# Kernel optimization log

Measured on AMD Instinct MI355X. Metric: run time of the kernel, lower is better.

The kernel has to match this reference:

```python
import jax, jax.numpy as jnp
import numpy as np

N = 100_000      # nodes
E = 1_600_000    # edges
IN = 128         # input_dim
HID = 64         # hidden_dim
H = 4            # num_heads
DH = HID // H    # per-head dim
L = 3            # num_layers
OUT = 64         # output_dim
SLOPE = 0.2      # DGL GATConv LeakyReLU default
EPS = 1e-5       # LayerNorm eps


def setup_inputs() -> dict:
    key = jax.random.key(0)
    ks = jax.random.split(key, 20)
    s = 0.02
    return {
        "node_features": jax.random.normal(ks[0], (N, IN), jnp.float32),
        "src": jax.random.randint(ks[1], (E,), 0, N, jnp.int32),
        "dst": jax.random.randint(ks[2], (E,), 0, N, jnp.int32),
        # input projection
        "W_in": jax.random.normal(ks[3], (IN, HID), jnp.float32) * s,
        "b_in": jnp.zeros((HID,), jnp.float32),
        # rewiring MLP: Linear(2*HID,64) -> Tanh -> Linear(64,1) -> Sigmoid
        "W_a1": jax.random.normal(ks[4], (2 * HID, 64), jnp.float32) * s,
        "b_a1": jnp.zeros((64,), jnp.float32),
        "W_a2": jax.random.normal(ks[5], (64, 1), jnp.float32) * s,
        "b_a2": jnp.zeros((1,), jnp.float32),
        # stacked GATConv params for L layers
        "W_gat": jax.random.normal(ks[6], (L, HID, H * DH), jnp.float32) * s,
        "a_l": jax.random.normal(ks[7], (L, H, DH), jnp.float32) * s,
        "a_r": jax.random.normal(ks[8], (L, H, DH), jnp.float32) * s,
        "b_gat": jnp.zeros((L, H, DH), jnp.float32),
        # LayerNorm + output projection
        "ln_g": jnp.ones((HID,), jnp.float32),
        "ln_b": jnp.zeros((HID,), jnp.float32),
        "W_out": jax.random.normal(ks[9], (HID, OUT), jnp.float32) * s,
        "b_out": jnp.zeros((OUT,), jnp.float32),
    }


def _gat_layer(h, src, dst, W, al, ar, b):
    # h: (N, HID) -> z: (N, H, DH)
    z = (h @ W).reshape(N, H, DH)
    el = jnp.sum(z * al, axis=-1)                       # (N, H)
    er = jnp.sum(z * ar, axis=-1)                       # (N, H)
    e = jax.nn.leaky_relu(el[src] + er[dst], SLOPE)     # (E, H)
    # segment softmax over incoming edges of each dst node
    m = jax.ops.segment_max(e, dst, num_segments=N)     # (N, H)
    ex = jnp.exp(e - m[dst])                            # (E, H)
    den = jax.ops.segment_sum(ex, dst, num_segments=N)  # (N, H)
    alpha = ex / den[dst]                               # (E, H)
    msg = z[src] * alpha[..., None]                     # (E, H, DH)
    out = jax.ops.segment_sum(msg, dst, num_segments=N) # (N, H, DH)
    # residual (identity since HID == H*DH) + bias, then flatten(1)
    out = out + h.reshape(N, H, DH) + b
    return out.reshape(N, H * DH)


def reference(node_features, src, dst, W_in, b_in, W_a1, b_a1, W_a2, b_a2,
              W_gat, a_l, a_r, b_gat, ln_g, ln_b, W_out, b_out):
    h = node_features @ W_in + b_in                     # (N, HID)
    # GraphRewiringModule: edge-wise gather + MLP + sigmoid score
    he = jnp.concatenate([h[src], h[dst]], axis=1)      # (E, 2*HID)
    edge_score = jax.nn.sigmoid(jnp.tanh(he @ W_a1 + b_a1) @ W_a2 + b_a2)  # (E,1); unused downstream, as in source
    for l in range(L):
        h = _gat_layer(h, src, dst, W_gat[l], a_l[l], a_r[l], b_gat[l])
    # LayerNorm
    mu = jnp.mean(h, axis=-1, keepdims=True)
    var = jnp.mean((h - mu) ** 2, axis=-1, keepdims=True)
    h = (h - mu) * jax.lax.rsqrt(var + EPS) * ln_g + ln_b
    return h @ W_out + b_out                            # (N, OUT)
```

## Files before the change

kernel.cpp:

```cpp
#include <hip/hip_runtime.h>

#define NN 100000
#define EE 1600000
#define IN_DIM 128
#define HID 64
#define NH 4
#define DH 16
#define NL 3
#define OUT_DIM 64
#define SLOPE 0.2f
#define LN_EPS 1e-5f
#define RB 4
#define ZSC 64.0f
#define ZISC 0.015625f

#define BSH 9
#define BSZ 512
#define NB ((NN + BSZ - 1) / BSZ)
#define CAP 10240
#define CHUNK 4096
#define P1_BLOCKS ((EE + CHUNK - 1) / CHUNK)

using short8 = __attribute__((ext_vector_type(8))) short;
using f32x4  = __attribute__((ext_vector_type(4))) float;
using f32x2  = __attribute__((ext_vector_type(2))) float;

__device__ __forceinline__ float bcast(float x, int lane) {
    return __int_as_float(__builtin_amdgcn_readlane(__float_as_int(x), lane));
}
__device__ __forceinline__ unsigned f2bf(float x) {
    unsigned u = __float_as_uint(x);
    u += 0x7FFFu + ((u >> 16) & 1u);
    return u >> 16;
}
__device__ __forceinline__ float bf2f(unsigned short b) {
    return __uint_as_float(((unsigned)b) << 16);
}
__device__ __forceinline__ float bflo(unsigned zp) {
    return __uint_as_float(zp << 16);
}
__device__ __forceinline__ float bfhi(unsigned zp) {
    return __uint_as_float(zp & 0xFFFF0000u);
}

__global__ void k_wpack(const float* __restrict__ W, uint4* __restrict__ Wb) {
    const int tid = blockIdx.x * 256 + threadIdx.x;
    if (tid >= 1024) return;
    const int lane = tid & 63;
    const int ntkk = tid >> 6;
    const int nt = ntkk & 3, kk = ntkk >> 2;
    const int k0 = kk * 32 + (lane >> 4) * 8;
    const int n  = nt * 16 + (lane & 15);
    unsigned dw[4];
#pragma unroll
    for (int p = 0; p < 4; ++p) {
        const unsigned lo = f2bf(W[(k0 + 2 * p) * HID + n]);
        const unsigned hi = f2bf(W[(k0 + 2 * p + 1) * HID + n]);
        dw[p] = lo | (hi << 16);
    }
    Wb[ntkk * 64 + lane] = make_uint4(dw[0], dw[1], dw[2], dw[3]);
}

__device__ float walv(const float* __restrict__ W, const float* __restrict__ al,
                      const float* __restrict__ ar, int k, int c) {
    if (c < 4) {
        float s = 0.f;
#pragma unroll
        for (int d = 0; d < 16; ++d) s += W[k * HID + c * 16 + d] * al[c * 16 + d];
        return s;
    }
    if (c < 8) {
        const int hh = c - 4;
        float s = 0.f;
#pragma unroll
        for (int d = 0; d < 16; ++d) s += W[k * HID + hh * 16 + d] * ar[hh * 16 + d];
        return s;
    }
    return 0.f;
}

__global__ void k_wpack_gat(const float* __restrict__ W_gat, const float* __restrict__ a_l,
                            const float* __restrict__ a_r, uint4* __restrict__ Wbg) {
    const int l = blockIdx.y;
    const int tid = blockIdx.x * 256 + threadIdx.x;
    if (tid >= 640) return;
    const int lane = tid & 63;
    const int f = tid >> 6;
    const int kk = f / 5, nt = f % 5;
    const float* W  = W_gat + (size_t)l * HID * HID;
    const float* al = a_l + (size_t)l * HID;
    const float* ar = a_r + (size_t)l * HID;
    const int k0 = kk * 32 + (lane >> 4) * 8;
    const int n  = lane & 15;
    unsigned dw[4];
#pragma unroll
    for (int p = 0; p < 4; ++p) {
        float b0, b1;
        if (nt < 4) {
            b0 = W[(k0 + 2 * p) * HID + nt * 16 + n];
            b1 = W[(k0 + 2 * p + 1) * HID + nt * 16 + n];
        } else {
            b0 = walv(W, al, ar, k0 + 2 * p, n);
            b1 = walv(W, al, ar, k0 + 2 * p + 1, n);
        }
        dw[p] = f2bf(b0) | (f2bf(b1) << 16);
    }
    Wbg[(size_t)l * 640 + f * 64 + lane] = make_uint4(dw[0], dw[1], dw[2], dw[3]);
}

__global__ __launch_bounds__(256)
void k_in_gemm(const float* __restrict__ X, const uint4* __restrict__ Wb,
               const float* __restrict__ b, unsigned* __restrict__ h32) {
    const int l  = threadIdx.x & 63;
    const int wv = threadIdx.x >> 6;
    const int wrow = blockIdx.x * 64 + wv * 16;
    if (wrow >= NN) return;
    const int arow = wrow + (l & 15);
    const int kb_off = (l >> 4) * 8;
    f32x4 acc[4];
#pragma unroll
    for (int nt = 0; nt < 4; ++nt) acc[nt] = (f32x4){0.f, 0.f, 0.f, 0.f};
    const float* xr = X + (size_t)arow * IN_DIM;
#pragma unroll
    for (int kk = 0; kk < 4; ++kk) {
        const int kb = kk * 32 + kb_off;
        const float4 xa = *(const float4*)(xr + kb);
        const float4 xb = *(const float4*)(xr + kb + 4);
        const unsigned d0 = f2bf(xa.x) | (f2bf(xa.y) << 16);
        const unsigned d1 = f2bf(xa.z) | (f2bf(xa.w) << 16);
        const unsigned d2 = f2bf(xb.x) | (f2bf(xb.y) << 16);
        const unsigned d3 = f2bf(xb.z) | (f2bf(xb.w) << 16);
        const uint4 au = make_uint4(d0, d1, d2, d3);
        const short8 af = __builtin_bit_cast(short8, au);
#pragma unroll
        for (int nt = 0; nt < 4; ++nt) {
            const uint4 bu = Wb[(kk * 4 + nt) * 64 + l];
            const short8 bf = __builtin_bit_cast(short8, bu);
            acc[nt] = __builtin_amdgcn_mfma_f32_16x16x32_bf16(af, bf, acc[nt], 0, 0, 0);
        }
    }
    const int grp = l >> 4, ci = l & 15;
#pragma unroll
    for (int nt = 0; nt < 4; ++nt) {
        const float bv = b[nt * 16 + ci];
#pragma unroll
        for (int r = 0; r < 4; ++r) {
            const int row = wrow + grp * 4 + r;
            const unsigned my = f2bf(acc[nt][r] + bv);
            const unsigned ot = (unsigned)__shfl_xor((int)my, 1, 64);
            if ((ci & 1) == 0)
                h32[(size_t)row * 32 + nt * 8 + (ci >> 1)] = my | (ot << 16);
        }
    }
}

__global__ __launch_bounds__(256)
void k_zgemm(const unsigned short* __restrict__ h16, const uint4* __restrict__ Wbg,
             unsigned* __restrict__ zb8, float* __restrict__ el, float* __restrict__ er) {
    const int l  = threadIdx.x & 63;
    const int wv = threadIdx.x >> 6;
    const int wrow = blockIdx.x * 64 + wv * 16;
    if (wrow >= NN) return;
    const int arow = wrow + (l & 15);
    const int kb_off = (l >> 4) * 8;
    f32x4 acc[5];
#pragma unroll
    for (int nt = 0; nt < 5; ++nt) acc[nt] = (f32x4){0.f, 0.f, 0.f, 0.f};
#pragma unroll
    for (int kk = 0; kk < 2; ++kk) {
        const int kb = kk * 32 + kb_off;
        const uint4 au = *(const uint4*)(h16 + (size_t)arow * 64 + kb);
        const short8 af = __builtin_bit_cast(short8, au);
#pragma unroll
        for (int nt = 0; nt < 5; ++nt) {
            const uint4 bu = Wbg[(kk * 5 + nt) * 64 + l];
            const short8 bf = __builtin_bit_cast(short8, bu);
            acc[nt] = __builtin_amdgcn_mfma_f32_16x16x32_bf16(af, bf, acc[nt], 0, 0, 0);
        }
    }
    const int grp = l >> 4, ci = l & 15;
#pragma unroll
    for (int nt = 0; nt < 4; ++nt) {
#pragma unroll
        for (int r = 0; r < 4; ++r) {
            const int row = wrow + grp * 4 + r;
            const float v = acc[nt][r] * ZSC;
            const float vn = __shfl_xor(v, 1, 64);
            unsigned pk = (unsigned)__builtin_amdgcn_cvt_pk_fp8_f32(v, vn, 0, false) & 0xFFFFu;
            const unsigned pk2 = (unsigned)__shfl_xor((int)pk, 2, 64);
            pk |= pk2 << 16;
            if ((ci & 3) == 0)
                zb8[(size_t)row * 16 + nt * 4 + (ci >> 2)] = pk;
        }
    }
#pragma unroll
    for (int r = 0; r < 4; ++r) {
        const int row = wrow + grp * 4 + r;
        const float v = acc[4][r];
        if (ci < 4) el[row * NH + ci] = v;
        else if (ci < 8) er[row * NH + (ci - 4)] = v;
    }
}


__global__ void k_zero_bcnt(int* __restrict__ bcnt, int* __restrict__ esrc_pad) {
    if (threadIdx.x < NB) bcnt[threadIdx.x] = 0;
    if (threadIdx.x < 32) esrc_pad[threadIdx.x] = 0;
}

__global__ __launch_bounds__(256)
void k_bucketize(const int* __restrict__ src, const int* __restrict__ dst,
                 int* __restrict__ bcnt, unsigned* __restrict__ bbuf) {
    __shared__ int lh[256];
    __shared__ int lbase[256];
    __shared__ int lcnt[256];
    __shared__ int gbase[256];
    __shared__ int sc[256];
    __shared__ int2 stage[CHUNK];
    const int t = threadIdx.x;
    const int e0 = blockIdx.x * CHUNK;
    const int n = min(CHUNK, EE - e0);
    lh[t] = 0;
    __syncthreads();
    int myd[CHUNK / 256], mys[CHUNK / 256];
#pragma unroll
    for (int i = 0; i < CHUNK / 256; ++i) {
        const int o = i * 256 + t;
        if (o < n) {
            myd[i] = dst[e0 + o];
            mys[i] = src[e0 + o];
            atomicAdd(&lh[myd[i] >> BSH], 1);
        } else myd[i] = -1;
    }
    __syncthreads();
    {
        const int v = lh[t];
        lcnt[t] = v;
        sc[t] = v;
        __syncthreads();
        for (int off = 1; off < 256; off <<= 1) {
            const int x = (t >= off) ? sc[t - off] : 0;
            __syncthreads();
            sc[t] += x;
            __syncthreads();
        }
        lbase[t] = sc[t] - v;
        lh[t] = sc[t] - v;
    }
    __syncthreads();
#pragma unroll
    for (int i = 0; i < CHUNK / 256; ++i) {
        if (myd[i] >= 0) {
            const int b = myd[i] >> BSH;
            const int p = atomicAdd(&lh[b], 1);
            stage[p] = make_int2(mys[i], myd[i]);
        }
    }
    __syncthreads();
    if (t < NB && lcnt[t] > 0) gbase[t] = atomicAdd(&bcnt[t], lcnt[t]);
    __syncthreads();
    for (int i = t; i < n; i += 256) {
        const int2 en = stage[i];
        const int b = en.y >> BSH;
        const int gp = gbase[b] + (i - lbase[b]);
        if (gp < CAP)
            bbuf[(size_t)b * CAP + gp] =
                (unsigned)en.x | (((unsigned)en.y & 511u) << 17);
    }
}

__global__ void k_bscan(const int* __restrict__ bcnt, int* __restrict__ bbase,
                        int* __restrict__ rowptr) {
    const int t = threadIdx.x;
    __shared__ int sc[256];
    const int v = (t < NB) ? bcnt[t] : 0;
    sc[t] = v;
    __syncthreads();
    for (int off = 1; off < 256; off <<= 1) {
        const int x = (t >= off) ? sc[t - off] : 0;
        __syncthreads();
        sc[t] += x;
        __syncthreads();
    }
    if (t < NB) bbase[t] = sc[t] - v;
    if (t == 0) rowptr[NN] = EE;
}

__global__ __launch_bounds__(256)
void k_localcsr(const int* __restrict__ bcnt, const int* __restrict__ bbase,
                const unsigned* __restrict__ bbuf, int* __restrict__ rowptr,
                int* __restrict__ esrc) {
    const int b = blockIdx.x;
    const int t = threadIdx.x;
    const int cnt = bcnt[b];
    const int base = bbase[b];
    const int n0 = b * BSZ;
    const int nn = min(BSZ, NN - n0);
    __shared__ int lh[BSZ];
    __shared__ int lsc[BSZ];
    __shared__ int sc[256];
    for (int i = t; i < BSZ; i += 256) lh[i] = 0;
    __syncthreads();
    const unsigned* bb = bbuf + (size_t)b * CAP;
    for (int i = t; i < cnt; i += 256) atomicAdd(&lh[(bb[i] >> 17) & 511u], 1);
    __syncthreads();
    const int a0 = lh[2 * t], a1 = lh[2 * t + 1];
    const int ts = a0 + a1;
    sc[t] = ts;
    __syncthreads();
    for (int off = 1; off < 256; off <<= 1) {
        const int x = (t >= off) ? sc[t - off] : 0;
        __syncthreads();
        sc[t] += x;
        __syncthreads();
    }
    const int ebase = sc[t] - ts;
    lsc[2 * t] = ebase;
    lsc[2 * t + 1] = ebase + a0;
    __syncthreads();
    for (int i = t; i < BSZ; i += 256) {
        if (i < nn) rowptr[n0 + i] = base + lsc[i];
        lh[i] = lsc[i];
    }
    __syncthreads();
    for (int i = t; i < cnt; i += 256) {
        const unsigned en = bb[i];
        const int p = atomicAdd(&lh[(en >> 17) & 511u], 1);
        esrc[base + p] = (int)(en & 0x1FFFFu);
    }
}

__global__ __launch_bounds__(256)
void k_gat_dst(const int* __restrict__ rowptr, const int* __restrict__ esrc,
               const float* __restrict__ el, const float* __restrict__ er,
               const uint2* __restrict__ zb64, const unsigned short* __restrict__ hin16,
               const float* __restrict__ bg, unsigned* __restrict__ hout32) {
    const int j  = threadIdx.x & 63;
    const int wv = threadIdx.x >> 6;
    const int d = blockIdx.x * 4 + wv;
    if (d >= NN) return;
    const int g = j >> 3;
    const int q = j & 7;
    const int hh = q >> 1;
    const int r0 = rowptr[d], r1 = rowptr[d + 1];
    const float erh = er[d * NH + hh];
    uint4 hv4 = make_uint4(0, 0, 0, 0);
    if (g == 0) hv4 = *(const uint4*)(hin16 + (size_t)d * 64 + 8 * q);
    float a0 = 0.f, a1 = 0.f, a2 = 0.f, a3 = 0.f;
    float a4 = 0.f, a5 = 0.f, a6 = 0.f, a7 = 0.f;
    float den = 0.f;
    unsigned sA = (unsigned)esrc[r0 + g];
    float avA = el[sA * NH + hh];
    uint2 zpA = zb64[sA * 8u + q];
    unsigned sB = (unsigned)esrc[r0 + 8 + g];
    for (int i = r0; i < r1; i += 8) {
        const float avB = el[sB * NH + hh];
        const uint2 zpB = zb64[sB * 8u + q];
        const unsigned sC = (unsigned)esrc[i + 16 + g];
        const float x = avA + erh;
        float w = __expf(fmaxf(x, SLOPE * x));
        w = (i + g < r1) ? w : 0.f;
        den += w;
        const f32x2 p0 = __builtin_amdgcn_cvt_pk_f32_fp8(zpA.x, false);
        const f32x2 p1 = __builtin_amdgcn_cvt_pk_f32_fp8(zpA.x, true);
        const f32x2 p2 = __builtin_amdgcn_cvt_pk_f32_fp8(zpA.y, false);
        const f32x2 p3 = __builtin_amdgcn_cvt_pk_f32_fp8(zpA.y, true);
        a0 = fmaf(w, p0.x, a0);
        a1 = fmaf(w, p0.y, a1);
        a2 = fmaf(w, p1.x, a2);
        a3 = fmaf(w, p1.y, a3);
        a4 = fmaf(w, p2.x, a4);
        a5 = fmaf(w, p2.y, a5);
        a6 = fmaf(w, p3.x, a6);
        a7 = fmaf(w, p3.y, a7);
        sA = sB; avA = avB; zpA = zpB; sB = sC;
    }
#pragma unroll
    for (int m = 8; m <= 32; m <<= 1) {
        den += __shfl_xor(den, m, 64);
        a0 += __shfl_xor(a0, m, 64);
        a1 += __shfl_xor(a1, m, 64);
        a2 += __shfl_xor(a2, m, 64);
        a3 += __shfl_xor(a3, m, 64);
        a4 += __shfl_xor(a4, m, 64);
        a5 += __shfl_xor(a5, m, 64);
        a6 += __shfl_xor(a6, m, 64);
        a7 += __shfl_xor(a7, m, 64);
    }
    if (g == 0) {
        const int c = 8 * q;
        float o0 = bflo(hv4.x) + bg[c + 0], o1 = bfhi(hv4.x) + bg[c + 1];
        float o2 = bflo(hv4.y) + bg[c + 2], o3 = bfhi(hv4.y) + bg[c + 3];
        float o4 = bflo(hv4.z) + bg[c + 4], o5 = bfhi(hv4.z) + bg[c + 5];
        float o6 = bflo(hv4.w) + bg[c + 6], o7 = bfhi(hv4.w) + bg[c + 7];
        if (r1 > r0) {
            const float rds = (1.f / den) * ZISC;
            o0 = fmaf(a0, rds, o0); o1 = fmaf(a1, rds, o1);
            o2 = fmaf(a2, rds, o2); o3 = fmaf(a3, rds, o3);
            o4 = fmaf(a4, rds, o4); o5 = fmaf(a5, rds, o5);
            o6 = fmaf(a6, rds, o6); o7 = fmaf(a7, rds, o7);
        }
        const uint4 ov = make_uint4(f2bf(o0) | (f2bf(o1) << 16),
                                    f2bf(o2) | (f2bf(o3) << 16),
                                    f2bf(o4) | (f2bf(o5) << 16),
                                    f2bf(o6) | (f2bf(o7) << 16));
        *(uint4*)(hout32 + (size_t)d * 32 + 4 * q) = ov;
    }
}

__global__ __launch_bounds__(256, 4)
void k_ln_out(const unsigned short* __restrict__ h16, const float* __restrict__ g,
              const float* __restrict__ be, const float* __restrict__ Wo,
              const float* __restrict__ bo, float* __restrict__ out) {
    const int j = threadIdx.x & 63;
    float Wreg[HID];
#pragma unroll
    for (int k = 0; k < HID; ++k) Wreg[k] = Wo[k * OUT_DIM + j];
    const float gj = g[j], bej = be[j], boj = bo[j];
    const int wid = (blockIdx.x * blockDim.x + threadIdx.x) >> 6;
    const int nw  = (gridDim.x * blockDim.x) >> 6;
    for (int v0 = wid * RB; v0 < NN; v0 += nw * RB) {
        float hn[RB];
#pragma unroll
        for (int r = 0; r < RB; ++r) {
            const float x = bf2f(h16[(size_t)(v0 + r) * HID + j]);
            float s = x;
#pragma unroll
            for (int m = 32; m >= 1; m >>= 1) s += __shfl_xor(s, m, 64);
            const float mu = s * (1.f / 64.f);
            const float dx = x - mu;
            float vs = dx * dx;
#pragma unroll
            for (int m = 32; m >= 1; m >>= 1) vs += __shfl_xor(vs, m, 64);
            hn[r] = dx * rsqrtf(vs * (1.f / 64.f) + LN_EPS) * gj + bej;
        }
        float acc[RB];
#pragma unroll
        for (int r = 0; r < RB; ++r) acc[r] = boj;
#pragma unroll
        for (int k = 0; k < HID; ++k) {
#pragma unroll
            for (int r = 0; r < RB; ++r)
                acc[r] = fmaf(bcast(hn[r], k), Wreg[k], acc[r]);
        }
#pragma unroll
        for (int r = 0; r < RB; ++r) out[(size_t)(v0 + r) * OUT_DIM + j] = acc[r];
    }
}

extern "C" void kernel_launch(void* const* d_in, const int* in_sizes, int n_in,
                              void* d_out, int out_size, void* d_ws, size_t ws_size,
                              hipStream_t stream) {
    const float* X     = (const float*)d_in[0];
    const int*   src   = (const int*)d_in[1];
    const int*   dst   = (const int*)d_in[2];
    const float* W_in  = (const float*)d_in[3];
    const float* b_in  = (const float*)d_in[4];
    const float* W_gat = (const float*)d_in[9];
    const float* a_l   = (const float*)d_in[10];
    const float* a_r   = (const float*)d_in[11];
    const float* b_gat = (const float*)d_in[12];
    const float* ln_g  = (const float*)d_in[13];
    const float* ln_b  = (const float*)d_in[14];
    const float* W_out = (const float*)d_in[15];
    const float* b_out = (const float*)d_in[16];
    float* out = (float*)d_out;

    char* ws = (char*)d_ws;
    unsigned short* hA16 = (unsigned short*)ws;
    unsigned short* hB16 = hA16 + (size_t)NN * HID;
    unsigned* zb8 = (unsigned*)(hB16 + (size_t)NN * HID);
    float* el = (float*)(zb8 + (size_t)NN * 16);
    float* er = el + (size_t)NN * NH;
    int* rowptr = (int*)(er + (size_t)NN * NH);
    int* esrc   = rowptr + NN + 1;
    int* bcnt   = esrc + EE + 32;
    int* bbase  = bcnt + NB;
    uintptr_t wp = (uintptr_t)(bbase + NB);
    wp = (wp + 15) & ~(uintptr_t)15;
    uint4* Wb   = (uint4*)wp;
    uint4* Wbg  = Wb + 1024;
    unsigned* bbuf = (unsigned*)hB16;

    k_wpack<<<4, 256, 0, stream>>>(W_in, Wb);
    k_wpack_gat<<<dim3(3, NL), 256, 0, stream>>>(W_gat, a_l, a_r, Wbg);
    k_in_gemm<<<(NN + 63) / 64, 256, 0, stream>>>(X, Wb, b_in, (unsigned*)hA16);

    k_zero_bcnt<<<1, 256, 0, stream>>>(bcnt, esrc + EE);
    k_bucketize<<<P1_BLOCKS, 256, 0, stream>>>(src, dst, bcnt, bbuf);
    k_bscan<<<1, 256, 0, stream>>>(bcnt, bbase, rowptr);
    k_localcsr<<<NB, 256, 0, stream>>>(bcnt, bbase, bbuf, rowptr, esrc);

    unsigned short* hin = hA16;
    unsigned short* hout = hB16;
    for (int l = 0; l < NL; ++l) {
        k_zgemm<<<(NN + 63) / 64, 256, 0, stream>>>(hin, Wbg + (size_t)l * 640,
                                                    zb8, el, er);
        k_gat_dst<<<(NN + 3) / 4, 256, 0, stream>>>(rowptr, esrc, el, er,
                                                    (const uint2*)zb8, hin,
                                                    b_gat + (size_t)l * HID,
                                                    (unsigned*)hout);
        unsigned short* t = hin; hin = hout; hout = t;
    }

    k_ln_out<<<1024, 256, 0, stream>>>(hin, ln_g, ln_b, W_out, b_out, out);
}
```

Before: 296.0 us.

## Recompute source attention logits from fp8 z in gather; shrink bucketize staging

The GAT aggregation kernel no longer gathers a precomputed el value per edge. It recomputes el inside the edge loop as a dot product of the already-loaded fp8 z row with a_l, plus one lane shuffle. This removes one random 4-byte gather per edge and the el writes from the z-GEMM. The cost is extra ALU work per edge, and el is now computed from quantized fp8 z instead of the fp32 GEMM output, which lowers accuracy. Separately, the bucketize staging buffer stores the packed 32-bit edge word plus a byte-sized bucket id instead of an int2, cutting LDS use.

```diff
diff --git a/kernel.cpp b/kernel.cpp
--- a/kernel.cpp
+++ b/kernel.cpp
@@ -156,7 +156,7 @@
 
 __global__ __launch_bounds__(256)
 void k_zgemm(const unsigned short* __restrict__ h16, const uint4* __restrict__ Wbg,
-             unsigned* __restrict__ zb8, float* __restrict__ el, float* __restrict__ er) {
+             unsigned* __restrict__ zb8, float* __restrict__ er) {
     const int l  = threadIdx.x & 63;
     const int wv = threadIdx.x >> 6;
     const int wrow = blockIdx.x * 64 + wv * 16;
@@ -197,8 +197,7 @@
     for (int r = 0; r < 4; ++r) {
         const int row = wrow + grp * 4 + r;
         const float v = acc[4][r];
-        if (ci < 4) el[row * NH + ci] = v;
-        else if (ci < 8) er[row * NH + (ci - 4)] = v;
+        if (ci >= 4 && ci < 8) er[row * NH + (ci - 4)] = v;
     }
 }
 
@@ -216,7 +215,8 @@
     __shared__ int lcnt[256];
     __shared__ int gbase[256];
     __shared__ int sc[256];
-    __shared__ int2 stage[CHUNK];
+    __shared__ unsigned stage[CHUNK];
+    __shared__ unsigned char sbkt[CHUNK];
     const int t = threadIdx.x;
     const int e0 = blockIdx.x * CHUNK;
     const int n = min(CHUNK, EE - e0);
@@ -253,19 +253,17 @@
         if (myd[i] >= 0) {
             const int b = myd[i] >> BSH;
             const int p = atomicAdd(&lh[b], 1);
-            stage[p] = make_int2(mys[i], myd[i]);
+            stage[p] = (unsigned)mys[i] | (((unsigned)myd[i] & 511u) << 17);
+            sbkt[p] = (unsigned char)b;
         }
     }
     __syncthreads();
     if (t < NB && lcnt[t] > 0) gbase[t] = atomicAdd(&bcnt[t], lcnt[t]);
     __syncthreads();
     for (int i = t; i < n; i += 256) {
-        const int2 en = stage[i];
-        const int b = en.y >> BSH;
+        const int b = sbkt[i];
         const int gp = gbase[b] + (i - lbase[b]);
-        if (gp < CAP)
-            bbuf[(size_t)b * CAP + gp] =
-                (unsigned)en.x | (((unsigned)en.y & 511u) << 17);
+        if (gp < CAP) bbuf[(size_t)b * CAP + gp] = stage[i];
     }
 }
 
@@ -332,7 +330,7 @@
 
 __global__ __launch_bounds__(256)
 void k_gat_dst(const int* __restrict__ rowptr, const int* __restrict__ esrc,
-               const float* __restrict__ el, const float* __restrict__ er,
+               const float* __restrict__ al, const float* __restrict__ er,
                const uint2* __restrict__ zb64, const unsigned short* __restrict__ hin16,
                const float* __restrict__ bg, unsigned* __restrict__ hout32) {
     const int j  = threadIdx.x & 63;
@@ -344,27 +342,30 @@
     const int hh = q >> 1;
     const int r0 = rowptr[d], r1 = rowptr[d + 1];
     const float erh = er[d * NH + hh];
+    const float4 alA = *(const float4*)(al + 8 * q);
+    const float4 alB = *(const float4*)(al + 8 * q + 4);
     uint4 hv4 = make_uint4(0, 0, 0, 0);
     if (g == 0) hv4 = *(const uint4*)(hin16 + (size_t)d * 64 + 8 * q);
     float a0 = 0.f, a1 = 0.f, a2 = 0.f, a3 = 0.f;
     float a4 = 0.f, a5 = 0.f, a6 = 0.f, a7 = 0.f;
     float den = 0.f;
     unsigned sA = (unsigned)esrc[r0 + g];
-    float avA = el[sA * NH + hh];
     uint2 zpA = zb64[sA * 8u + q];
     unsigned sB = (unsigned)esrc[r0 + 8 + g];
     for (int i = r0; i < r1; i += 8) {
-        const float avB = el[sB * NH + hh];
         const uint2 zpB = zb64[sB * 8u + q];
         const unsigned sC = (unsigned)esrc[i + 16 + g];
-        const float x = avA + erh;
-        float w = __expf(fmaxf(x, SLOPE * x));
-        w = (i + g < r1) ? w : 0.f;
-        den += w;
         const f32x2 p0 = __builtin_amdgcn_cvt_pk_f32_fp8(zpA.x, false);
         const f32x2 p1 = __builtin_amdgcn_cvt_pk_f32_fp8(zpA.x, true);
         const f32x2 p2 = __builtin_amdgcn_cvt_pk_f32_fp8(zpA.y, false);
         const f32x2 p3 = __builtin_amdgcn_cvt_pk_f32_fp8(zpA.y, true);
+        float dot = p0.x * alA.x + p0.y * alA.y + p1.x * alA.z + p1.y * alA.w
+                  + p2.x * alB.x + p2.y * alB.y + p3.x * alB.z + p3.y * alB.w;
+        dot += __shfl_xor(dot, 1, 64);
+        const float x = dot * ZISC + erh;
+        float w = __expf(fmaxf(x, SLOPE * x));
+        w = (i + g < r1) ? w : 0.f;
+        den += w;
         a0 = fmaf(w, p0.x, a0);
         a1 = fmaf(w, p0.y, a1);
         a2 = fmaf(w, p1.x, a2);
@@ -373,7 +374,7 @@
         a5 = fmaf(w, p2.y, a5);
         a6 = fmaf(w, p3.x, a6);
         a7 = fmaf(w, p3.y, a7);
-        sA = sB; avA = avB; zpA = zpB; sB = sC;
+        sA = sB; zpA = zpB; sB = sC;
     }
 #pragma unroll
     for (int m = 8; m <= 32; m <<= 1) {
@@ -470,8 +471,7 @@
     unsigned short* hA16 = (unsigned short*)ws;
     unsigned short* hB16 = hA16 + (size_t)NN * HID;
     unsigned* zb8 = (unsigned*)(hB16 + (size_t)NN * HID);
-    float* el = (float*)(zb8 + (size_t)NN * 16);
-    float* er = el + (size_t)NN * NH;
+    float* er = (float*)(zb8 + (size_t)NN * 16);
     int* rowptr = (int*)(er + (size_t)NN * NH);
     int* esrc   = rowptr + NN + 1;
     int* bcnt   = esrc + EE + 32;
@@ -495,8 +495,9 @@
     unsigned short* hout = hB16;
     for (int l = 0; l < NL; ++l) {
         k_zgemm<<<(NN + 63) / 64, 256, 0, stream>>>(hin, Wbg + (size_t)l * 640,
-                                                    zb8, el, er);
-        k_gat_dst<<<(NN + 3) / 4, 256, 0, stream>>>(rowptr, esrc, el, er,
+                                                    zb8, er);
+        k_gat_dst<<<(NN + 3) / 4, 256, 0, stream>>>(rowptr, esrc,
+                                                    a_l + (size_t)l * HID, er,
                                                     (const uint2*)zb8, hin,
                                                     b_gat + (size_t)l * HID,
                                                     (unsigned*)hout);
```

Measured after the change: 296.2 us. Within noise of the previous version (+0.1%).
